# Kernel tuning notes

Hardware: AMD Instinct MI355X
Metric: run time of the kernel (lower is better)

The kernel has to match this reference:

```python
import jax, jax.numpy as jnp
import numpy as np

BLOCK_SIZE = 64


def setup_inputs() -> dict:
    key = jax.random.key(0)
    kq, kk, kv, km = jax.random.split(key, 4)
    H, N, D = 16, 8192, 64
    nb = N // BLOCK_SIZE
    return {
        "q": jax.random.normal(kq, (H, N, D), dtype=jnp.float32),
        "k": jax.random.normal(kk, (H, N, D), dtype=jnp.float32),
        "v": jax.random.normal(kv, (H, N, D), dtype=jnp.float32),
        "block_mask": jax.random.randint(km, (nb, nb), 0, 2, dtype=jnp.int32),
    }


def reference(q, k, v, block_mask):
    """Block-sparse flash attention with online softmax.

    q, k, v: [H, N, D]; block_mask: [N//B, N//B] (1 = valid, 0 = masked).
    Scans over key blocks, processing all query rows at once; masked blocks
    contribute exactly zero (exp(-inf) = 0), matching the original's skip.
    """
    H, N, D = q.shape
    B = BLOCK_SIZE
    nb = N // B
    scale = D ** -0.5

    kb = k.reshape(H, nb, B, D).transpose(1, 0, 2, 3)  # [nb, H, B, D]
    vb = v.reshape(H, nb, B, D).transpose(1, 0, 2, 3)  # [nb, H, B, D]
    mask_cols = block_mask.T  # [nb_key, nb_query]: row j = validity of key block j per query block

    m0 = jnp.full((H, N, 1), -jnp.inf, dtype=q.dtype)
    l0 = jnp.zeros((H, N, 1), dtype=q.dtype)
    o0 = jnp.zeros((H, N, D), dtype=q.dtype)

    def step(carry, xs):
        m, l, o = carry
        k_j, v_j, mcol = xs  # k_j/v_j: [H, B, D]; mcol: [nb] over query blocks
        logits = jnp.einsum('hnd,hbd->hnb', q, k_j) * scale  # [H, N, B]
        valid = (jnp.repeat(mcol, B) > 0)[None, :, None]      # [1, N, 1]
        logits = jnp.where(valid, logits, -jnp.inf)
        m_new = jnp.maximum(m, logits.max(-1, keepdims=True))
        # guard: if everything so far is masked, m_new = -inf; use 0 to keep exps finite (=0)
        m_safe = jnp.where(jnp.isneginf(m_new), jnp.zeros_like(m_new), m_new)
        a_old = jnp.exp(m - m_safe)       # rescale of previous accumulators
        p = jnp.exp(logits - m_safe)      # masked entries -> 0
        l = a_old * l + p.sum(-1, keepdims=True)
        o = a_old * o + jnp.einsum('hnb,hbd->hnd', p, v_j)
        return (m_new, l, o), None

    (m, l, o), _ = jax.lax.scan(step, (m0, l0, o0), (kb, vb, mask_cols))
    return o / l
```

## Files before the change

### kernel.cpp

```cpp
#include <hip/hip_runtime.h>
#include <hip/hip_bf16.h>

#define Hh 16
#define Nn 8192
#define Dd 64
#define NB 128

typedef float  f32x4   __attribute__((ext_vector_type(4)));
typedef float  f32x16  __attribute__((ext_vector_type(16)));
typedef float  float4_ __attribute__((ext_vector_type(4)));
typedef short  bf16x8  __attribute__((ext_vector_type(8)));
typedef unsigned short ushort8  __attribute__((ext_vector_type(8)));
typedef unsigned short ushort4_ __attribute__((ext_vector_type(4)));

typedef const __attribute__((address_space(1))) unsigned int gu32;
typedef __attribute__((address_space(3))) unsigned int lu32;

#define QSCALE 0.1803368801111244f

__device__ __forceinline__ unsigned short f2bf(float f) {
    union { float f; unsigned u; } x; x.f = f;
    unsigned r = x.u + 0x7fffu + ((x.u >> 16) & 1u);
    return (unsigned short)(r >> 16);
}

__device__ __forceinline__ unsigned packbf2(float lo, float hi) {
    __hip_bfloat162 h2 = __float22bfloat162_rn(make_float2(lo, hi));
    unsigned u; __builtin_memcpy(&u, &h2, 4);
    return u;
}

__global__ void cvt_k(const float* __restrict__ k, unsigned short* __restrict__ ko) {
    int i = blockIdx.x * 256 + threadIdx.x;
    float4_ b = ((const float4_*)k)[i];
    ushort4_ ob;
#pragma unroll
    for (int j = 0; j < 4; ++j) ob[j] = f2bf(b[j]);
    ((ushort4_*)ko)[i] = ob;
}

__global__ void cvt_vt(const float* __restrict__ v, unsigned short* __restrict__ vt) {
    int jb = blockIdx.x, h = blockIdx.y, t = threadIdx.x;
    __shared__ float T[64][65];
    const float4_* src = (const float4_*)(v + ((long)h * Nn + jb * 64) * Dd);
#pragma unroll
    for (int it = 0; it < 4; ++it) {
        int r = (t >> 4) + it * 16;
        int c0 = (t & 15) * 4;
        float4_ x = src[r * 16 + (t & 15)];
#pragma unroll
        for (int i2 = 0; i2 < 4; ++i2) T[c0 + i2][r] = x[i2];
    }
    __syncthreads();
    int d = t >> 2, seg = (t & 3) * 16;
    ushort8 o0, o1;
#pragma unroll
    for (int i2 = 0; i2 < 8; ++i2) o0[i2] = f2bf(T[d][seg + i2]);
#pragma unroll
    for (int i2 = 0; i2 < 8; ++i2) o1[i2] = f2bf(T[d][seg + 8 + i2]);
    unsigned short* dst = vt + (((size_t)h * NB + jb) * Dd + d) * 64 + seg;
    *(ushort8*)dst = o0;
    *(ushort8*)(dst + 8) = o1;
}

__global__ __launch_bounds__(256, 4) void attn32(
        const unsigned short* __restrict__ k16,
        const unsigned short* __restrict__ vt16,
        const float* __restrict__ qf,
        const int* __restrict__ mask,
        float* __restrict__ out) {
    int bid = blockIdx.x;
    int h = (bid & 7) | ((bid >> 9) << 3);
    int qb2 = (bid >> 3) & 63;
    int tid = threadIdx.x;
    int wid = tid >> 6, l = tid & 63;
    int q5 = l & 31, hi = l >> 5;
    int pair = wid >> 1;
    int kvrole = wid & 1;
    int half = wid >> 1;

    __shared__ unsigned short Kl[2][4096];
    __shared__ unsigned short Vl[2][4096];

    const int* mrowA = mask + (qb2 * 2) * NB;
    const int* mrowB = mask + (qb2 * 2 + 1) * NB;
    unsigned long long a_lo = __ballot(mrowA[l] != 0);
    unsigned long long a_hi = __ballot(mrowA[64 + l] != 0);
    unsigned long long c_lo = __ballot(mrowB[l] != 0);
    unsigned long long c_hi = __ballot(mrowB[64 + l] != 0);
    unsigned long long u_lo = a_lo | c_lo, u_hi = a_hi | c_hi;
    int ucount = __popcll(u_lo) + __popcll(u_hi);

    if (ucount == 0) {
        float4_ z = {0.f, 0.f, 0.f, 0.f};
        float4_* ob = (float4_*)(out + ((size_t)h * Nn + qb2 * 128) * Dd);
        for (int x = tid; x < 128 * 64 / 4; x += 256) ob[x] = z;
        return;
    }

    unsigned long long own_lo = pair ? c_lo : a_lo;
    unsigned long long own_hi = pair ? c_hi : a_hi;
    int own_count = __popcll(own_lo) + __popcll(own_hi);

    size_t qrow = (size_t)h * Nn + qb2 * 128 + pair * 64 + (wid & 1) * 32 + q5;
    bf16x8 qfrag[4];
#pragma unroll
    for (int ds_ = 0; ds_ < 4; ++ds_) {
        const float4_* qs = (const float4_*)(qf + qrow * Dd + ds_ * 16 + hi * 8);
        float4_ x = qs[0], y = qs[1];
        union { unsigned u[4]; bf16x8 v; } u;
        u.u[0] = packbf2(x[0] * QSCALE, x[1] * QSCALE);
        u.u[1] = packbf2(x[2] * QSCALE, x[3] * QSCALE);
        u.u[2] = packbf2(y[0] * QSCALE, y[1] * QSCALE);
        u.u[3] = packbf2(y[2] * QSCALE, y[3] * QSCALE);
        qfrag[ds_] = u.v;
    }

    union { unsigned short s[8]; bf16x8 v; } ones;
#pragma unroll
    for (int i2 = 0; i2 < 8; ++i2) ones.s[i2] = 0x3F80;

    const unsigned short* sp[4];
#pragma unroll
    for (int ff = 0; ff < 4; ++ff) {
        int f = half * 4 + ff;
        if (kvrole == 0)
            sp[ff] = k16 + (size_t)h * (Nn * Dd)
                   + (size_t)(q5 + 32 * (f >> 2)) * Dd + (f & 3) * 16 + hi * 8;
        else
            sp[ff] = vt16 + (size_t)h * (Nn * Dd)
                   + (size_t)(q5 + 32 * (f >> 2)) * 64 + (f & 3) * 16 + hi * 8;
    }
    const int jmul = 64 * Dd;

    unsigned long long r0 = u_lo, r1 = u_hi;
    auto next_j = [&]() {
        int jj;
        if (r0) { jj = __ffsll(r0) - 1; r0 &= r0 - 1; }
        else    { jj = 63 + __ffsll(r1); r1 &= r1 - 1; }
        return jj;
    };

    auto issue = [&](int nbuf, int jj) {
        unsigned short* lb = (kvrole == 0) ? &Kl[nbuf][0] : &Vl[nbuf][0];
#pragma unroll
        for (int ff = 0; ff < 4; ++ff) {
            const unsigned short* g = sp[ff] + (size_t)jj * jmul;
            __builtin_amdgcn_global_load_lds((gu32*)g,
                (lu32*)(lb + (half * 4 + ff) * 512), 16, 0, 0);
        }
    };

    int jcur = next_j();
    issue(0, jcur);

    f32x16 o0 = {}, o1 = {}, ls = {};

    for (int i = 0; i < ucount; ++i) {
        int buf = i & 1;
        __syncthreads();
        int jnext = 0;
        if (i + 1 < ucount) { jnext = next_j(); issue(buf ^ 1, jnext); }

        bool act = (jcur < 64) ? ((own_lo >> jcur) & 1ull)
                               : ((own_hi >> (jcur - 64)) & 1ull);
        unsigned msk = act ? 0xFFFFFFFFu : 0u;
        jcur = jnext;

        const char* kb = (const char*)Kl + buf * 8192 + l * 16;
        const char* vb = (const char*)Vl + buf * 8192 + l * 16;

        f32x16 s0 = {}, s1 = {};
#pragma unroll
        for (int ds_ = 0; ds_ < 4; ++ds_) {
            bf16x8 kf0 = *(const bf16x8*)(kb + ds_ * 1024);
            s0 = __builtin_amdgcn_mfma_f32_32x32x16_bf16(kf0, qfrag[ds_], s0, 0, 0, 0);
        }
#pragma unroll
        for (int ds_ = 0; ds_ < 4; ++ds_) {
            bf16x8 kf1 = *(const bf16x8*)(kb + 4096 + ds_ * 1024);
            s1 = __builtin_amdgcn_mfma_f32_32x32x16_bf16(kf1, qfrag[ds_], s1, 0, 0, 0);
        }

#pragma unroll
        for (int e = 0; e < 16; ++e) s0[e] = __builtin_amdgcn_exp2f(s0[e]);
#pragma unroll
        for (int e = 0; e < 16; ++e) s1[e] = __builtin_amdgcn_exp2f(s1[e]);

        unsigned w0[8], w1[8];
#pragma unroll
        for (int jj = 0; jj < 8; ++jj) {
            w0[jj] = packbf2(s0[2 * jj], s0[2 * jj + 1]) & msk;
            w1[jj] = packbf2(s1[2 * jj], s1[2 * jj + 1]) & msk;
        }
        auto swap32 = [&](unsigned& a, unsigned& b) {
            unsigned send = hi ? a : b;
            unsigned recv = (unsigned)__shfl_xor((int)send, 32);
            a = hi ? recv : a;
            b = hi ? b : recv;
        };
        swap32(w0[0], w0[2]); swap32(w0[1], w0[3]);
        swap32(w0[4], w0[6]); swap32(w0[5], w0[7]);
        swap32(w1[0], w1[2]); swap32(w1[1], w1[3]);
        swap32(w1[4], w1[6]); swap32(w1[5], w1[7]);

        union U { unsigned u[4]; bf16x8 v; };
        U pbs[4];
        pbs[0].u[0] = w0[0]; pbs[0].u[1] = w0[1]; pbs[0].u[2] = w0[2]; pbs[0].u[3] = w0[3];
        pbs[1].u[0] = w0[4]; pbs[1].u[1] = w0[5]; pbs[1].u[2] = w0[6]; pbs[1].u[3] = w0[7];
        pbs[2].u[0] = w1[0]; pbs[2].u[1] = w1[1]; pbs[2].u[2] = w1[2]; pbs[2].u[3] = w1[3];
        pbs[3].u[0] = w1[4]; pbs[3].u[1] = w1[5]; pbs[3].u[2] = w1[6]; pbs[3].u[3] = w1[7];

#pragma unroll
        for (int c = 0; c < 4; ++c) {
            bf16x8 vf0 = *(const bf16x8*)(vb + c * 1024);
            o0 = __builtin_amdgcn_mfma_f32_32x32x16_bf16(vf0, pbs[c].v, o0, 0, 0, 0);
        }
#pragma unroll
        for (int c = 0; c < 4; ++c) {
            bf16x8 vf1 = *(const bf16x8*)(vb + 4096 + c * 1024);
            o1 = __builtin_amdgcn_mfma_f32_32x32x16_bf16(vf1, pbs[c].v, o1, 0, 0, 0);
        }
#pragma unroll
        for (int c = 0; c < 4; ++c)
            ls = __builtin_amdgcn_mfma_f32_32x32x16_bf16(ones.v, pbs[c].v, ls, 0, 0, 0);
    }

    float inv = own_count ? (1.0f / ls[0]) : 0.f;
    float* obase = out + qrow * Dd;
#pragma unroll
    for (int s4 = 0; s4 < 4; ++s4) {
        float4_ t0, t1;
#pragma unroll
        for (int e = 0; e < 4; ++e) { t0[e] = o0[4 * s4 + e] * inv; t1[e] = o1[4 * s4 + e] * inv; }
        *(float4_*)(obase + 8 * s4 + 4 * hi)      = t0;
        *(float4_*)(obase + 32 + 8 * s4 + 4 * hi) = t1;
    }
}

__global__ void attn_main(const float* __restrict__ qf, const float* __restrict__ kf,
                          const float* __restrict__ vf, const int* __restrict__ mask,
                          float* __restrict__ out) {
    int id = blockIdx.x;
    int h = id & 15, qb = id >> 4;
    int tid = threadIdx.x;
    int lane = tid & 63, wid = tid >> 6;
    int l15 = lane & 15, l4 = lane >> 4;

    __shared__ unsigned short Kl[2][64 * 64];
    __shared__ unsigned short Vl[2][64 * 64];
    __shared__ unsigned short Pl[4][16 * 64];

    const int* mrow = mask + qb * NB;
    unsigned long long b0 = __ballot(mrow[lane] != 0);
    unsigned long long b1 = __ballot(mrow[64 + lane] != 0);
    int count = __popcll(b0) + __popcll(b1);

    float* op = out + ((long)h * Nn + qb * 64 + wid * 16) * Dd;

    if (count == 0) {
#pragma unroll
        for (int r = 0; r < 4; ++r)
#pragma unroll
            for (int dn = 0; dn < 4; ++dn)
                op[(l4 * 4 + r) * Dd + dn * 16 + l15] = 0.f;
        return;
    }

    long qrow = (long)h * Nn + qb * 64 + wid * 16 + l15;
    bf16x8 qfrag[2];
#pragma unroll
    for (int dc = 0; dc < 2; ++dc) {
        const float4_* qs = (const float4_*)qf + qrow * 16 + dc * 8 + l4 * 2;
        float4_ x = qs[0], y = qs[1];
        union { unsigned short s[8]; bf16x8 v; } u;
#pragma unroll
        for (int i2 = 0; i2 < 4; ++i2) {
            u.s[i2] = f2bf(x[i2] * 0.125f);
            u.s[4 + i2] = f2bf(y[i2] * 0.125f);
        }
        qfrag[dc] = u.v;
    }

    int sgq = tid & 7;
    int srow = tid >> 3;
    float4_ kf4[2][2]; float4_ vf4[4];
    int vk = tid & 63, vd0 = (tid >> 6) * 16;

    auto load_kv = [&](int j) {
        const float4_* ks = (const float4_*)kf + ((long)h * Nn + j * 64) * 16;
#pragma unroll
        for (int it = 0; it < 2; ++it) {
            kf4[it][0] = ks[(srow + it * 32) * 16 + sgq * 2];
            kf4[it][1] = ks[(srow + it * 32) * 16 + sgq * 2 + 1];
        }
        const float4_* vs = (const float4_*)vf + ((long)h * Nn + j * 64) * 16;
#pragma unroll
        for (int c = 0; c < 4; ++c) vf4[c] = vs[vk * 16 + (vd0 >> 2) + c];
    };

    auto write_kv = [&](int buf) {
#pragma unroll
        for (int it = 0; it < 2; ++it) {
            int r = srow + it * 32;
            union { unsigned short s[8]; ushort8 v; } u;
#pragma unroll
            for (int i2 = 0; i2 < 4; ++i2) {
                u.s[i2] = f2bf(kf4[it][0][i2]);
                u.s[4 + i2] = f2bf(kf4[it][1][i2]);
            }
            *(ushort8*)((char*)&Kl[buf][0] + r * 128 + (((sgq ^ r) & 7) << 4)) = u.v;
        }
#pragma unroll
        for (int i2 = 0; i2 < 16; ++i2) {
            int d = vd0 + i2;
            *((unsigned short*)((char*)&Vl[buf][0] + d * 128 +
                ((((vk >> 3) ^ d) & 7) << 4) + ((vk & 7) << 1))) = f2bf(vf4[i2 >> 2][i2 & 3]);
        }
    };

    f32x4 o_acc[4] = {};
    float m_r[4], l_r[4];
#pragma unroll
    for (int r = 0; r < 4; ++r) { m_r[r] = -INFINITY; l_r[r] = 0.f; }

    unsigned long long r0 = b0, r1 = b1;
    auto next_j = [&]() {
        int jj;
        if (r0) { jj = __ffsll(r0) - 1; r0 &= r0 - 1; }
        else    { jj = 63 + __ffsll(r1); r1 &= r1 - 1; }
        return jj;
    };

    load_kv(next_j());

    for (int i = 0; i < count; ++i) {
        int buf = i & 1;
        write_kv(buf);
        __syncthreads();
        if (i + 1 < count) load_kv(next_j());

        f32x4 s[4] = {};
#pragma unroll
        for (int dc = 0; dc < 2; ++dc) {
#pragma unroll
            for (int kn = 0; kn < 4; ++kn) {
                int krow = kn * 16 + l15;
                bf16x8 kfr = *(const bf16x8*)((const char*)&Kl[buf][0] +
                               krow * 128 + ((((l4 + dc * 4) ^ krow) & 7) << 4));
                s[kn] = __builtin_amdgcn_mfma_f32_16x16x32_bf16(qfrag[dc], kfr, s[kn], 0, 0, 0);
            }
        }

#pragma unroll
        for (int r = 0; r < 4; ++r) {
            float mx = fmaxf(fmaxf(s[0][r], s[1][r]), fmaxf(s[2][r], s[3][r]));
#pragma unroll
            for (int off = 1; off < 16; off <<= 1) mx = fmaxf(mx, __shfl_xor(mx, off));
            float mn = fmaxf(m_r[r], mx);
            float a = __expf(m_r[r] - mn);
            m_r[r] = mn;
            float psum = 0.f;
#pragma unroll
            for (int kn = 0; kn < 4; ++kn) { float p = __expf(s[kn][r] - mn); s[kn][r] = p; psum += p; }
#pragma unroll
            for (int off = 1; off < 16; off <<= 1) psum += __shfl_xor(psum, off);
            l_r[r] = l_r[r] * a + psum;
            o_acc[0][r] *= a; o_acc[1][r] *= a; o_acc[2][r] *= a; o_acc[3][r] *= a;
        }

#pragma unroll
        for (int kn = 0; kn < 4; ++kn) {
#pragma unroll
            for (int r = 0; r < 4; ++r) {
                int prow = l4 * 4 + r;
                int pc = kn * 16 + l15;
                *((unsigned short*)((char*)&Pl[wid][0] + prow * 128 +
                    ((((pc >> 3) ^ prow) & 7) << 4) + ((pc & 7) << 1))) = f2bf(s[kn][r]);
            }
        }

        bf16x8 pa[2];
#pragma unroll
        for (int kc = 0; kc < 2; ++kc)
            pa[kc] = *(const bf16x8*)((const char*)&Pl[wid][0] +
                      l15 * 128 + ((((l4 + kc * 4) ^ l15) & 7) << 4));
#pragma unroll
        for (int dn = 0; dn < 4; ++dn) {
            int vrow = dn * 16 + l15;
#pragma unroll
            for (int kc = 0; kc < 2; ++kc) {
                bf16x8 vbf = *(const bf16x8*)((const char*)&Vl[buf][0] +
                             vrow * 128 + ((((l4 + kc * 4) ^ vrow) & 7) << 4));
                o_acc[dn] = __builtin_amdgcn_mfma_f32_16x16x32_bf16(pa[kc], vbf, o_acc[dn], 0, 0, 0);
            }
        }
    }

#pragma unroll
    for (int r = 0; r < 4; ++r) {
        float inv = 1.0f / l_r[r];
#pragma unroll
        for (int dn = 0; dn < 4; ++dn)
            op[(l4 * 4 + r) * Dd + dn * 16 + l15] = o_acc[dn][r] * inv;
    }
}

extern "C" void kernel_launch(void* const* d_in, const int* in_sizes, int n_in,
                              void* d_out, int out_size, void* d_ws, size_t ws_size,
                              hipStream_t stream) {
    const float* q = (const float*)d_in[0];
    const float* k = (const float*)d_in[1];
    const float* v = (const float*)d_in[2];
    const int* mask = (const int*)d_in[3];
    float* out = (float*)d_out;

    size_t elems = (size_t)Hh * Nn * Dd;
    size_t need = 2 * elems * sizeof(unsigned short);
    if (ws_size >= need) {
        unsigned short* k16 = (unsigned short*)d_ws;
        unsigned short* vt16 = k16 + elems;
        cvt_k<<<dim3((unsigned)(elems / 1024)), 256, 0, stream>>>(k, k16);
        cvt_vt<<<dim3(NB, Hh), 256, 0, stream>>>(v, vt16);
        attn32<<<dim3(Hh * NB / 2), 256, 0, stream>>>(k16, vt16, q, mask, out);
    } else {
        attn_main<<<dim3(Hh * NB), 256, 0, stream>>>(q, k, v, mask, out);
    }
}
```

Measured before the change: 313.6 us.

## Give each query-block pair its own KV stream over its own mask bits

Each wave pair (one 64-row query block) now streams only the key blocks that are valid for its own mask row, using separate double-buffered K/V LDS tiles per pair. Previously both pairs walked the union of their masks and zeroed out the inactive blocks. The loop now runs max(cntA, cntB) iterations, and a pair that has finished its own blocks issues dummy loads and masks its output. This removes wasted MFMA and exp work on blocks masked for one pair, at the cost of twice the LDS (32KB) and launch bounds lowered from 4 to 2 blocks per CU.

```diff
diff --git a/kernel.cpp b/kernel.cpp
--- a/kernel.cpp
+++ b/kernel.cpp
@@ -63,7 +63,7 @@
     *(ushort8*)(dst + 8) = o1;
 }
 
-__global__ __launch_bounds__(256, 4) void attn32(
+__global__ __launch_bounds__(256, 2) void attn32(
         const unsigned short* __restrict__ k16,
         const unsigned short* __restrict__ vt16,
         const float* __restrict__ qf,
@@ -77,10 +77,9 @@
     int q5 = l & 31, hi = l >> 5;
     int pair = wid >> 1;
     int kvrole = wid & 1;
-    int half = wid >> 1;
-
-    __shared__ unsigned short Kl[2][4096];
-    __shared__ unsigned short Vl[2][4096];
+
+    __shared__ unsigned short Kl[2][2][4096];
+    __shared__ unsigned short Vl[2][2][4096];
 
     const int* mrowA = mask + (qb2 * 2) * NB;
     const int* mrowB = mask + (qb2 * 2 + 1) * NB;
@@ -88,21 +87,22 @@
     unsigned long long a_hi = __ballot(mrowA[64 + l] != 0);
     unsigned long long c_lo = __ballot(mrowB[l] != 0);
     unsigned long long c_hi = __ballot(mrowB[64 + l] != 0);
-    unsigned long long u_lo = a_lo | c_lo, u_hi = a_hi | c_hi;
-    int ucount = __popcll(u_lo) + __popcll(u_hi);
-
-    if (ucount == 0) {
+    int cntA = __popcll(a_lo) + __popcll(a_hi);
+    int cntB = __popcll(c_lo) + __popcll(c_hi);
+    int maxcnt = cntA > cntB ? cntA : cntB;
+
+    if (maxcnt == 0) {
         float4_ z = {0.f, 0.f, 0.f, 0.f};
         float4_* ob = (float4_*)(out + ((size_t)h * Nn + qb2 * 128) * Dd);
         for (int x = tid; x < 128 * 64 / 4; x += 256) ob[x] = z;
         return;
     }
 
-    unsigned long long own_lo = pair ? c_lo : a_lo;
-    unsigned long long own_hi = pair ? c_hi : a_hi;
-    int own_count = __popcll(own_lo) + __popcll(own_hi);
-
-    size_t qrow = (size_t)h * Nn + qb2 * 128 + pair * 64 + (wid & 1) * 32 + q5;
+    int cnt_own = pair ? cntB : cntA;
+    unsigned long long r0 = pair ? c_lo : a_lo;
+    unsigned long long r1 = pair ? c_hi : a_hi;
+
+    size_t qrow = (size_t)h * Nn + qb2 * 128 + pair * 64 + kvrole * 32 + q5;
     bf16x8 qfrag[4];
 #pragma unroll
     for (int ds_ = 0; ds_ < 4; ++ds_) {
@@ -120,55 +120,48 @@
 #pragma unroll
     for (int i2 = 0; i2 < 8; ++i2) ones.s[i2] = 0x3F80;
 
-    const unsigned short* sp[4];
-#pragma unroll
-    for (int ff = 0; ff < 4; ++ff) {
-        int f = half * 4 + ff;
+    const unsigned short* sp[8];
+#pragma unroll
+    for (int f = 0; f < 8; ++f) {
         if (kvrole == 0)
-            sp[ff] = k16 + (size_t)h * (Nn * Dd)
-                   + (size_t)(q5 + 32 * (f >> 2)) * Dd + (f & 3) * 16 + hi * 8;
+            sp[f] = k16 + (size_t)h * (Nn * Dd)
+                  + (size_t)(q5 + 32 * (f >> 2)) * Dd + (f & 3) * 16 + hi * 8;
         else
-            sp[ff] = vt16 + (size_t)h * (Nn * Dd)
-                   + (size_t)(q5 + 32 * (f >> 2)) * 64 + (f & 3) * 16 + hi * 8;
+            sp[f] = vt16 + (size_t)h * (Nn * Dd)
+                  + (size_t)(q5 + 32 * (f >> 2)) * 64 + (f & 3) * 16 + hi * 8;
     }
     const int jmul = 64 * Dd;
 
-    unsigned long long r0 = u_lo, r1 = u_hi;
     auto next_j = [&]() {
         int jj;
-        if (r0) { jj = __ffsll(r0) - 1; r0 &= r0 - 1; }
-        else    { jj = 63 + __ffsll(r1); r1 &= r1 - 1; }
+        if (r0)      { jj = __ffsll(r0) - 1; r0 &= r0 - 1; }
+        else if (r1) { jj = 63 + __ffsll(r1); r1 &= r1 - 1; }
+        else         { jj = 0; }
         return jj;
     };
 
     auto issue = [&](int nbuf, int jj) {
-        unsigned short* lb = (kvrole == 0) ? &Kl[nbuf][0] : &Vl[nbuf][0];
-#pragma unroll
-        for (int ff = 0; ff < 4; ++ff) {
-            const unsigned short* g = sp[ff] + (size_t)jj * jmul;
-            __builtin_amdgcn_global_load_lds((gu32*)g,
-                (lu32*)(lb + (half * 4 + ff) * 512), 16, 0, 0);
+        unsigned short* lb = (kvrole == 0) ? &Kl[pair][nbuf][0] : &Vl[pair][nbuf][0];
+#pragma unroll
+        for (int f = 0; f < 8; ++f) {
+            const unsigned short* g = sp[f] + (size_t)jj * jmul;
+            __builtin_amdgcn_global_load_lds((gu32*)g, (lu32*)(lb + f * 512), 16, 0, 0);
         }
     };
 
-    int jcur = next_j();
-    issue(0, jcur);
+    issue(0, next_j());
 
     f32x16 o0 = {}, o1 = {}, ls = {};
 
-    for (int i = 0; i < ucount; ++i) {
+    for (int i = 0; i < maxcnt; ++i) {
         int buf = i & 1;
         __syncthreads();
-        int jnext = 0;
-        if (i + 1 < ucount) { jnext = next_j(); issue(buf ^ 1, jnext); }
-
-        bool act = (jcur < 64) ? ((own_lo >> jcur) & 1ull)
-                               : ((own_hi >> (jcur - 64)) & 1ull);
-        unsigned msk = act ? 0xFFFFFFFFu : 0u;
-        jcur = jnext;
-
-        const char* kb = (const char*)Kl + buf * 8192 + l * 16;
-        const char* vb = (const char*)Vl + buf * 8192 + l * 16;
+        if (i + 1 < maxcnt) issue(buf ^ 1, next_j());
+
+        unsigned msk = (i < cnt_own) ? 0xFFFFFFFFu : 0u;
+
+        const char* kb = (const char*)&Kl[pair][buf][0] + l * 16;
+        const char* vb = (const char*)&Vl[pair][buf][0] + l * 16;
 
         f32x16 s0 = {}, s1 = {};
 #pragma unroll
@@ -226,7 +219,7 @@
             ls = __builtin_amdgcn_mfma_f32_32x32x16_bf16(ones.v, pbs[c].v, ls, 0, 0, 0);
     }
 
-    float inv = own_count ? (1.0f / ls[0]) : 0.f;
+    float inv = cnt_own ? (1.0f / ls[0]) : 0.f;
     float* obase = out + qrow * Dd;
 #pragma unroll
     for (int s4 = 0; s4 < 4; ++s4) {
```

Measured after the change: 288.9 us (median of 3 runs). -7.9%, faster.
